# Kernel tuning notes

Hardware: AMD Instinct MI355X
Metric: run time of the kernel (lower is better)

## Reference

```python
import jax, jax.numpy as jnp
import numpy as np

N, E, D = 10000, 160000, 512


def setup_inputs() -> dict:
    key = jax.random.key(0)
    ks = jax.random.split(key, 5)
    x = jax.random.normal(ks[0], (N, D), dtype=jnp.float32)
    edge_index = jax.random.randint(ks[1], (2, E), 0, N, dtype=jnp.int32)
    W = jax.random.normal(ks[2], (D, D), dtype=jnp.float32) * (1.0 / np.sqrt(D))
    a_src = jax.random.normal(ks[3], (D,), dtype=jnp.float32) * 0.1
    a_dst = jax.random.normal(ks[4], (D,), dtype=jnp.float32) * 0.1
    bias = jnp.zeros((D,), dtype=jnp.float32)
    return {"x": x, "edge_index": edge_index, "W": W,
            "a_src": a_src, "a_dst": a_dst, "bias": bias}


def reference(x, edge_index, W, a_src, a_dst, bias):
    n = x.shape[0]
    # PyG GATConv default: add self-loops
    loops = jnp.arange(n, dtype=edge_index.dtype)
    src = jnp.concatenate([edge_index[0], loops])  # [E+N]
    dst = jnp.concatenate([edge_index[1], loops])  # [E+N]

    h = x @ W.T                                    # [N, D] linear projection
    e_src = h @ a_src                              # [N]
    e_dst = h @ a_dst                              # [N]
    e = e_src[src] + e_dst[dst]                    # [E+N]
    neg_slope = 0.2
    e = jnp.where(e > 0, e, neg_slope * e)         # leaky_relu

    # per-destination softmax (stable); self-loops guarantee non-empty segments
    m = jax.ops.segment_max(e, dst, num_segments=n)
    e = jnp.exp(e - m[dst])
    s = jax.ops.segment_sum(e, dst, num_segments=n)
    alpha = e / s[dst]                             # [E+N]

    msg = alpha[:, None] * h[src]                  # [E+N, D]
    out = jax.ops.segment_sum(msg, dst, num_segments=n) + bias  # [N, D]

    # module forward: x + elu(gat(x, edge_index))
    return x + jax.nn.elu(out)
```

## Files before the change

### kernel.cpp

```cpp
#include <hip/hip_runtime.h>
#include <hip/hip_bf16.h>

using bf16x8 = __attribute__((ext_vector_type(8))) __bf16;
using f32x4  = __attribute__((ext_vector_type(4))) float;

#define DFEAT 512
#define SLOTS 64

static __device__ __forceinline__ unsigned short f2bfbits(float f) {
    union { float f; unsigned int u; } v; v.f = f;
    unsigned int u = v.u;
    unsigned int r = (u + 0x7fffu + ((u >> 16) & 1u)) >> 16;
    return (unsigned short)r;
}

__global__ __launch_bounds__(256) void cvt_scatter_kernel(
    const float* __restrict__ x, const float* __restrict__ w,
    unsigned short* __restrict__ Xb, unsigned short* __restrict__ Wb,
    const int* __restrict__ srcv, const int* __restrict__ dstv,
    int* __restrict__ cur, int* __restrict__ slot,
    int nx4, int ntot4, int E, int T)
{
    int i = blockIdx.x * 256 + threadIdx.x;
    if (i < ntot4) {
        const float* in = (i < nx4) ? x : w;
        unsigned short* o = (i < nx4) ? Xb : Wb;
        int j = (i < nx4) ? i : i - nx4;
        float4 v = ((const float4*)in)[j];
        ushort4 u;
        u.x = f2bfbits(v.x); u.y = f2bfbits(v.y);
        u.z = f2bfbits(v.z); u.w = f2bfbits(v.w);
        ((ushort4*)o)[j] = u;
    }
    if (i < T) {
        int s, d;
        if (i < E) { s = srcv[i]; d = dstv[i]; }
        else       { s = d = i - E; }
        int pos = atomicAdd(&cur[d], 1);
        if (pos < SLOTS) slot[(size_t)d * SLOTS + pos] = s;
    }
}

__global__ __launch_bounds__(256, 2) void gemm_h_kernel(
    const unsigned short* __restrict__ X, const unsigned short* __restrict__ Wm,
    const float* __restrict__ avs, const float* __restrict__ avd,
    unsigned short* __restrict__ H, float* __restrict__ es, float* __restrict__ ed,
    int N)
{
    __shared__ unsigned short Bl[64 * 512];

    int L = blockIdx.x;
    int xcd = L & 7;
    int j   = L >> 3;
    int rpan = (j >> 3) * 8 + xcd;
    int cpan = j & 7;
    int rowPanels = (N + 127) >> 7;
    if (rpan >= rowPanels) return;
    int bm = rpan * 128;
    int bn = cpan * 64;

    int tid  = threadIdx.x;
    int wave = tid >> 6;
    int lane = tid & 63;
    int l15  = lane & 15;
    int quad = lane >> 4;

    for (int idx = tid; idx < 64 * 64; idx += 256) {
        int n = idx >> 6, c = idx & 63;
        uint4 v = *(const uint4*)(Wm + (size_t)(bn + n) * DFEAT + c * 8);
        int cs = c ^ (n & 7);
        *(uint4*)((char*)Bl + (size_t)n * 1024 + cs * 16) = v;
    }
    __syncthreads();

    int r0 = bm + wave * 32 + l15;
    int r1 = r0 + 16;
    int ra0 = r0 < N ? r0 : N - 1;
    int ra1 = r1 < N ? r1 : N - 1;
    const bf16x8* A0 = (const bf16x8*)(X + (size_t)ra0 * DFEAT);
    const bf16x8* A1 = (const bf16x8*)(X + (size_t)ra1 * DFEAT);
    const char* Bc = (const char*)Bl;
    int xorm = l15 & 7;
    int roff0 = (0 * 16 + l15) * 1024;
    int roff1 = (1 * 16 + l15) * 1024;
    int roff2 = (2 * 16 + l15) * 1024;
    int roff3 = (3 * 16 + l15) * 1024;

    f32x4 acc[2][4] = {};

    bf16x8 a0c = A0[quad],     a1c = A1[quad];
    bf16x8 a0n = A0[4 + quad], a1n = A1[4 + quad];
    bf16x8 b[4];
    {
        int cb = ((quad ^ xorm) * 16);
        b[0] = *(const bf16x8*)(Bc + roff0 + cb);
        b[1] = *(const bf16x8*)(Bc + roff1 + cb);
        b[2] = *(const bf16x8*)(Bc + roff2 + cb);
        b[3] = *(const bf16x8*)(Bc + roff3 + cb);
    }

    for (int k0 = 0; k0 < 16; ++k0) {
        int ka = ((k0 + 2 < 16 ? k0 + 2 : 15) * 4) + quad;
        bf16x8 a0f = A0[ka];
        bf16x8 a1f = A1[ka];
        int kb = ((k0 + 1 < 16 ? k0 + 1 : 15) * 4) + quad;
        int cb = (kb ^ xorm) * 16;
        bf16x8 bn0 = *(const bf16x8*)(Bc + roff0 + cb);
        bf16x8 bn1 = *(const bf16x8*)(Bc + roff1 + cb);
        bf16x8 bn2 = *(const bf16x8*)(Bc + roff2 + cb);
        bf16x8 bn3 = *(const bf16x8*)(Bc + roff3 + cb);
        acc[0][0] = __builtin_amdgcn_mfma_f32_16x16x32_bf16(a0c, b[0], acc[0][0], 0, 0, 0);
        acc[1][0] = __builtin_amdgcn_mfma_f32_16x16x32_bf16(a1c, b[0], acc[1][0], 0, 0, 0);
        acc[0][1] = __builtin_amdgcn_mfma_f32_16x16x32_bf16(a0c, b[1], acc[0][1], 0, 0, 0);
        acc[1][1] = __builtin_amdgcn_mfma_f32_16x16x32_bf16(a1c, b[1], acc[1][1], 0, 0, 0);
        acc[0][2] = __builtin_amdgcn_mfma_f32_16x16x32_bf16(a0c, b[2], acc[0][2], 0, 0, 0);
        acc[1][2] = __builtin_amdgcn_mfma_f32_16x16x32_bf16(a1c, b[2], acc[1][2], 0, 0, 0);
        acc[0][3] = __builtin_amdgcn_mfma_f32_16x16x32_bf16(a0c, b[3], acc[0][3], 0, 0, 0);
        acc[1][3] = __builtin_amdgcn_mfma_f32_16x16x32_bf16(a1c, b[3], acc[1][3], 0, 0, 0);
        a0c = a0n; a1c = a1n; a0n = a0f; a1n = a1f;
        b[0] = bn0; b[1] = bn1; b[2] = bn2; b[3] = bn3;
    }

    float as[4], ad[4];
    #pragma unroll
    for (int nt = 0; nt < 4; ++nt) {
        as[nt] = avs[bn + nt * 16 + l15];
        ad[nt] = avd[bn + nt * 16 + l15];
    }

    #pragma unroll
    for (int mt = 0; mt < 2; ++mt) {
        int rbase = bm + wave * 32 + mt * 16 + quad * 4;
        #pragma unroll
        for (int nt = 0; nt < 4; ++nt) {
            int col = bn + nt * 16 + l15;
            #pragma unroll
            for (int r = 0; r < 4; ++r) {
                int row = rbase + r;
                if (row < N) H[(size_t)row * DFEAT + col] = f2bfbits(acc[mt][nt][r]);
            }
        }
        #pragma unroll
        for (int r = 0; r < 4; ++r) {
            float ps = acc[mt][0][r] * as[0] + acc[mt][1][r] * as[1]
                     + acc[mt][2][r] * as[2] + acc[mt][3][r] * as[3];
            float pd = acc[mt][0][r] * ad[0] + acc[mt][1][r] * ad[1]
                     + acc[mt][2][r] * ad[2] + acc[mt][3][r] * ad[3];
            #pragma unroll
            for (int m = 1; m < 16; m <<= 1) {
                ps += __shfl_xor(ps, m);
                pd += __shfl_xor(pd, m);
            }
            int row = rbase + r;
            if (l15 == 0 && row < N) {
                atomicAdd(&es[row], ps);
                atomicAdd(&ed[row], pd);
            }
        }
    }
}

__global__ __launch_bounds__(256) void aggregate_kernel(
    const unsigned short* __restrict__ H, const float* __restrict__ x,
    const float* __restrict__ bias,
    const int* __restrict__ cur, const int* __restrict__ slot,
    const float* __restrict__ es, const float* __restrict__ ed,
    float* __restrict__ out, int N)
{
    int node = (blockIdx.x * 256 + threadIdx.x) >> 6;
    int lane = threadIdx.x & 63;
    if (node >= N) return;

    int k = cur[node];
    if (k > SLOTS) k = SLOTS;

    int   s = 0;
    float w = 0.f;
    if (lane < k) {
        s = slot[(size_t)node * SLOTS + lane];
        float e = es[s] + ed[node];
        e = e > 0.f ? e : 0.2f * e;
        w = __expf(e);
    }
    float denom = w;
    #pragma unroll
    for (int off = 32; off > 0; off >>= 1) denom += __shfl_xor(denom, off);
    float inv = 1.0f / denom;

    float a[8] = {};
    const unsigned short* Hl = H + lane * 8;

    auto accum = [&](int sj, float wj) {
        uint4 hv = *(const uint4*)(Hl + (size_t)sj * DFEAT);
        a[0] += wj * __uint_as_float(hv.x << 16);
        a[1] += wj * __uint_as_float(hv.x & 0xffff0000u);
        a[2] += wj * __uint_as_float(hv.y << 16);
        a[3] += wj * __uint_as_float(hv.y & 0xffff0000u);
        a[4] += wj * __uint_as_float(hv.z << 16);
        a[5] += wj * __uint_as_float(hv.z & 0xffff0000u);
        a[6] += wj * __uint_as_float(hv.w << 16);
        a[7] += wj * __uint_as_float(hv.w & 0xffff0000u);
    };

    int j = 0;
    for (; j + 3 < k; j += 4) {
        int   s0 = __shfl(s, j),     s1 = __shfl(s, j + 1);
        int   s2 = __shfl(s, j + 2), s3 = __shfl(s, j + 3);
        float w0 = __shfl(w, j),     w1 = __shfl(w, j + 1);
        float w2 = __shfl(w, j + 2), w3 = __shfl(w, j + 3);
        uint4 h0 = *(const uint4*)(Hl + (size_t)s0 * DFEAT);
        uint4 h1 = *(const uint4*)(Hl + (size_t)s1 * DFEAT);
        uint4 h2 = *(const uint4*)(Hl + (size_t)s2 * DFEAT);
        uint4 h3 = *(const uint4*)(Hl + (size_t)s3 * DFEAT);
        a[0] += w0 * __uint_as_float(h0.x << 16);
        a[1] += w0 * __uint_as_float(h0.x & 0xffff0000u);
        a[2] += w0 * __uint_as_float(h0.y << 16);
        a[3] += w0 * __uint_as_float(h0.y & 0xffff0000u);
        a[4] += w0 * __uint_as_float(h0.z << 16);
        a[5] += w0 * __uint_as_float(h0.z & 0xffff0000u);
        a[6] += w0 * __uint_as_float(h0.w << 16);
        a[7] += w0 * __uint_as_float(h0.w & 0xffff0000u);
        a[0] += w1 * __uint_as_float(h1.x << 16);
        a[1] += w1 * __uint_as_float(h1.x & 0xffff0000u);
        a[2] += w1 * __uint_as_float(h1.y << 16);
        a[3] += w1 * __uint_as_float(h1.y & 0xffff0000u);
        a[4] += w1 * __uint_as_float(h1.z << 16);
        a[5] += w1 * __uint_as_float(h1.z & 0xffff0000u);
        a[6] += w1 * __uint_as_float(h1.w << 16);
        a[7] += w1 * __uint_as_float(h1.w & 0xffff0000u);
        a[0] += w2 * __uint_as_float(h2.x << 16);
        a[1] += w2 * __uint_as_float(h2.x & 0xffff0000u);
        a[2] += w2 * __uint_as_float(h2.y << 16);
        a[3] += w2 * __uint_as_float(h2.y & 0xffff0000u);
        a[4] += w2 * __uint_as_float(h2.z << 16);
        a[5] += w2 * __uint_as_float(h2.z & 0xffff0000u);
        a[6] += w2 * __uint_as_float(h2.w << 16);
        a[7] += w2 * __uint_as_float(h2.w & 0xffff0000u);
        a[0] += w3 * __uint_as_float(h3.x << 16);
        a[1] += w3 * __uint_as_float(h3.x & 0xffff0000u);
        a[2] += w3 * __uint_as_float(h3.y << 16);
        a[3] += w3 * __uint_as_float(h3.y & 0xffff0000u);
        a[4] += w3 * __uint_as_float(h3.z << 16);
        a[5] += w3 * __uint_as_float(h3.z & 0xffff0000u);
        a[6] += w3 * __uint_as_float(h3.w << 16);
        a[7] += w3 * __uint_as_float(h3.w & 0xffff0000u);
    }
    for (; j < k; ++j) accum(__shfl(s, j), __shfl(w, j));

    int c = lane * 8;
    float4 b0 = *(const float4*)(bias + c);
    float4 b1 = *(const float4*)(bias + c + 4);
    float4 x0 = *(const float4*)(x + (size_t)node * DFEAT + c);
    float4 x1 = *(const float4*)(x + (size_t)node * DFEAT + c + 4);
    float r[8];
    r[0] = a[0] * inv + b0.x; r[1] = a[1] * inv + b0.y;
    r[2] = a[2] * inv + b0.z; r[3] = a[3] * inv + b0.w;
    r[4] = a[4] * inv + b1.x; r[5] = a[5] * inv + b1.y;
    r[6] = a[6] * inv + b1.z; r[7] = a[7] * inv + b1.w;
    #pragma unroll
    for (int i = 0; i < 8; ++i)
        r[i] = r[i] > 0.f ? r[i] : __expf(r[i]) - 1.f;
    float4 o0 = make_float4(x0.x + r[0], x0.y + r[1], x0.z + r[2], x0.w + r[3]);
    float4 o1 = make_float4(x1.x + r[4], x1.y + r[5], x1.z + r[6], x1.w + r[7]);
    *(float4*)(out + (size_t)node * DFEAT + c)     = o0;
    *(float4*)(out + (size_t)node * DFEAT + c + 4) = o1;
}

extern "C" void kernel_launch(void* const* d_in, const int* in_sizes, int n_in,
                              void* d_out, int out_size, void* d_ws, size_t ws_size,
                              hipStream_t stream)
{
    const float* x    = (const float*)d_in[0];
    const int*   edge = (const int*)d_in[1];
    const float* Wm   = (const float*)d_in[2];
    const float* avs  = (const float*)d_in[3];
    const float* avd  = (const float*)d_in[4];
    const float* bias = (const float*)d_in[5];

    const int D = DFEAT;
    const int N = in_sizes[0] / D;
    const int E = in_sizes[1] / 2;
    const int T = E + N;
    const int* srcv = edge;
    const int* dstv = edge + E;

    char* ws = (char*)d_ws;
    size_t off = 0;
    auto alloc = [&](size_t bytes) -> char* {
        char* p = ws + off;
        off += (bytes + 255) & ~(size_t)255;
        return p;
    };
    int*   cur  = (int*)alloc((size_t)N * 3 * 4);
    float* es   = (float*)(cur + N);
    float* ed   = es + N;
    int*   slot = (int*)alloc((size_t)N * SLOTS * 4);
    unsigned short* Xb = (unsigned short*)alloc((size_t)N * D * 2);
    unsigned short* Wb = (unsigned short*)alloc((size_t)D * D * 2);
    unsigned short* H  = (unsigned short*)alloc((size_t)N * D * 2);

    hipMemsetAsync(cur, 0, (size_t)N * 3 * 4, stream);

    int nx4   = (N * D) / 4;
    int ntot4 = nx4 + (D * D) / 4;
    int grid0 = (ntot4 > T ? ntot4 : T);
    cvt_scatter_kernel<<<dim3((grid0 + 255) / 256), 256, 0, stream>>>(
        x, Wm, Xb, Wb, srcv, dstv, cur, slot, nx4, ntot4, E, T);

    int rowPanels  = (N + 127) / 128;
    int rowPanels8 = ((rowPanels + 7) / 8) * 8;
    gemm_h_kernel<<<dim3(rowPanels8 * 8), 256, 0, stream>>>(
        Xb, Wb, avs, avd, H, es, ed, N);
    aggregate_kernel<<<dim3((N * 64 + 255) / 256), 256, 0, stream>>>(
        H, x, bias, cur, slot, es, ed, (float*)d_out, N);
}
```

Measured before the change: 144.8 us.

## Fuse bf16 conversion into GEMM and run edge scatter in extra GEMM blocks

Removes the separate convert/scatter kernel. The GEMM now reads fp32 X and W directly and converts them to bf16 in registers, so the bf16 staging copies of X and W are no longer written or read. The edge-slot scatter runs in extra blocks appended to the GEMM grid, which saves a launch and lets the atomics overlap with the matrix multiply. In exchange, the GEMM streams twice the bytes of A per tile, needs more registers to hold the fp32 prefetch buffers, and repeats the W conversion in every block.

```diff
diff --git a/kernel.cpp b/kernel.cpp
--- a/kernel.cpp
+++ b/kernel.cpp
@@ -14,42 +14,40 @@
     return (unsigned short)r;
 }
 
-__global__ __launch_bounds__(256) void cvt_scatter_kernel(
-    const float* __restrict__ x, const float* __restrict__ w,
-    unsigned short* __restrict__ Xb, unsigned short* __restrict__ Wb,
+static __device__ __forceinline__ bf16x8 cvt8(float4 u, float4 v) {
+    bf16x8 r;
+    r[0] = (__bf16)u.x; r[1] = (__bf16)u.y; r[2] = (__bf16)u.z; r[3] = (__bf16)u.w;
+    r[4] = (__bf16)v.x; r[5] = (__bf16)v.y; r[6] = (__bf16)v.z; r[7] = (__bf16)v.w;
+    return r;
+}
+
+__global__ __launch_bounds__(256, 2) void gemm_scatter_kernel(
+    const float* __restrict__ X, const float* __restrict__ Wf,
+    const float* __restrict__ avs, const float* __restrict__ avd,
+    unsigned short* __restrict__ H, float* __restrict__ es, float* __restrict__ ed,
     const int* __restrict__ srcv, const int* __restrict__ dstv,
     int* __restrict__ cur, int* __restrict__ slot,
-    int nx4, int ntot4, int E, int T)
-{
-    int i = blockIdx.x * 256 + threadIdx.x;
-    if (i < ntot4) {
-        const float* in = (i < nx4) ? x : w;
-        unsigned short* o = (i < nx4) ? Xb : Wb;
-        int j = (i < nx4) ? i : i - nx4;
-        float4 v = ((const float4*)in)[j];
-        ushort4 u;
-        u.x = f2bfbits(v.x); u.y = f2bfbits(v.y);
-        u.z = f2bfbits(v.z); u.w = f2bfbits(v.w);
-        ((ushort4*)o)[j] = u;
-    }
-    if (i < T) {
-        int s, d;
-        if (i < E) { s = srcv[i]; d = dstv[i]; }
-        else       { s = d = i - E; }
-        int pos = atomicAdd(&cur[d], 1);
-        if (pos < SLOTS) slot[(size_t)d * SLOTS + pos] = s;
-    }
-}
-
-__global__ __launch_bounds__(256, 2) void gemm_h_kernel(
-    const unsigned short* __restrict__ X, const unsigned short* __restrict__ Wm,
-    const float* __restrict__ avs, const float* __restrict__ avd,
-    unsigned short* __restrict__ H, float* __restrict__ es, float* __restrict__ ed,
-    int N)
+    int N, int E, int T, int Ggemm)
 {
     __shared__ unsigned short Bl[64 * 512];
 
     int L = blockIdx.x;
+    if (L >= Ggemm) {
+        int base = (L - Ggemm) * 1024 + threadIdx.x;
+        #pragma unroll
+        for (int t = 0; t < 4; ++t) {
+            int i = base + t * 256;
+            if (i < T) {
+                int s, d;
+                if (i < E) { s = srcv[i]; d = dstv[i]; }
+                else       { s = d = i - E; }
+                int pos = atomicAdd(&cur[d], 1);
+                if (pos < SLOTS) slot[(size_t)d * SLOTS + pos] = s;
+            }
+        }
+        return;
+    }
+
     int xcd = L & 7;
     int j   = L >> 3;
     int rpan = (j >> 3) * 8 + xcd;
@@ -67,9 +65,12 @@
 
     for (int idx = tid; idx < 64 * 64; idx += 256) {
         int n = idx >> 6, c = idx & 63;
-        uint4 v = *(const uint4*)(Wm + (size_t)(bn + n) * DFEAT + c * 8);
+        const float* wp = Wf + (size_t)(bn + n) * DFEAT + c * 8;
+        float4 u = *(const float4*)wp;
+        float4 v = *(const float4*)(wp + 4);
+        bf16x8 o = cvt8(u, v);
         int cs = c ^ (n & 7);
-        *(uint4*)((char*)Bl + (size_t)n * 1024 + cs * 16) = v;
+        *(bf16x8*)((char*)Bl + (size_t)n * 1024 + cs * 16) = o;
     }
     __syncthreads();
 
@@ -77,8 +78,8 @@
     int r1 = r0 + 16;
     int ra0 = r0 < N ? r0 : N - 1;
     int ra1 = r1 < N ? r1 : N - 1;
-    const bf16x8* A0 = (const bf16x8*)(X + (size_t)ra0 * DFEAT);
-    const bf16x8* A1 = (const bf16x8*)(X + (size_t)ra1 * DFEAT);
+    const float* A0p = X + (size_t)ra0 * DFEAT;
+    const float* A1p = X + (size_t)ra1 * DFEAT;
     const char* Bc = (const char*)Bl;
     int xorm = l15 & 7;
     int roff0 = (0 * 16 + l15) * 1024;
@@ -88,8 +89,15 @@
 
     f32x4 acc[2][4] = {};
 
-    bf16x8 a0c = A0[quad],     a1c = A1[quad];
-    bf16x8 a0n = A0[4 + quad], a1n = A1[4 + quad];
+    float4 c0u = *(const float4*)(A0p + quad * 8);
+    float4 c0v = *(const float4*)(A0p + quad * 8 + 4);
+    float4 c1u = *(const float4*)(A1p + quad * 8);
+    float4 c1v = *(const float4*)(A1p + quad * 8 + 4);
+    float4 n0u = *(const float4*)(A0p + (4 + quad) * 8);
+    float4 n0v = *(const float4*)(A0p + (4 + quad) * 8 + 4);
+    float4 n1u = *(const float4*)(A1p + (4 + quad) * 8);
+    float4 n1v = *(const float4*)(A1p + (4 + quad) * 8 + 4);
+
     bf16x8 b[4];
     {
         int cb = ((quad ^ xorm) * 16);
@@ -99,26 +107,55 @@
         b[3] = *(const bf16x8*)(Bc + roff3 + cb);
     }
 
-    for (int k0 = 0; k0 < 16; ++k0) {
-        int ka = ((k0 + 2 < 16 ? k0 + 2 : 15) * 4) + quad;
-        bf16x8 a0f = A0[ka];
-        bf16x8 a1f = A1[ka];
-        int kb = ((k0 + 1 < 16 ? k0 + 1 : 15) * 4) + quad;
-        int cb = (kb ^ xorm) * 16;
-        bf16x8 bn0 = *(const bf16x8*)(Bc + roff0 + cb);
-        bf16x8 bn1 = *(const bf16x8*)(Bc + roff1 + cb);
-        bf16x8 bn2 = *(const bf16x8*)(Bc + roff2 + cb);
-        bf16x8 bn3 = *(const bf16x8*)(Bc + roff3 + cb);
-        acc[0][0] = __builtin_amdgcn_mfma_f32_16x16x32_bf16(a0c, b[0], acc[0][0], 0, 0, 0);
-        acc[1][0] = __builtin_amdgcn_mfma_f32_16x16x32_bf16(a1c, b[0], acc[1][0], 0, 0, 0);
-        acc[0][1] = __builtin_amdgcn_mfma_f32_16x16x32_bf16(a0c, b[1], acc[0][1], 0, 0, 0);
-        acc[1][1] = __builtin_amdgcn_mfma_f32_16x16x32_bf16(a1c, b[1], acc[1][1], 0, 0, 0);
-        acc[0][2] = __builtin_amdgcn_mfma_f32_16x16x32_bf16(a0c, b[2], acc[0][2], 0, 0, 0);
-        acc[1][2] = __builtin_amdgcn_mfma_f32_16x16x32_bf16(a1c, b[2], acc[1][2], 0, 0, 0);
-        acc[0][3] = __builtin_amdgcn_mfma_f32_16x16x32_bf16(a0c, b[3], acc[0][3], 0, 0, 0);
-        acc[1][3] = __builtin_amdgcn_mfma_f32_16x16x32_bf16(a1c, b[3], acc[1][3], 0, 0, 0);
-        a0c = a0n; a1c = a1n; a0n = a0f; a1n = a1f;
-        b[0] = bn0; b[1] = bn1; b[2] = bn2; b[3] = bn3;
+    for (int k0 = 0; k0 < 16; k0 += 2) {
+        {
+            bf16x8 a0 = cvt8(c0u, c0v);
+            bf16x8 a1 = cvt8(c1u, c1v);
+            int ka = ((k0 + 2 < 16 ? k0 + 2 : 15) * 4 + quad) * 8;
+            c0u = *(const float4*)(A0p + ka);
+            c0v = *(const float4*)(A0p + ka + 4);
+            c1u = *(const float4*)(A1p + ka);
+            c1v = *(const float4*)(A1p + ka + 4);
+            int kb = (k0 + 1) * 4 + quad;
+            int cb = (kb ^ xorm) * 16;
+            bf16x8 bn0 = *(const bf16x8*)(Bc + roff0 + cb);
+            bf16x8 bn1 = *(const bf16x8*)(Bc + roff1 + cb);
+            bf16x8 bn2 = *(const bf16x8*)(Bc + roff2 + cb);
+            bf16x8 bn3 = *(const bf16x8*)(Bc + roff3 + cb);
+            acc[0][0] = __builtin_amdgcn_mfma_f32_16x16x32_bf16(a0, b[0], acc[0][0], 0, 0, 0);
+            acc[1][0] = __builtin_amdgcn_mfma_f32_16x16x32_bf16(a1, b[0], acc[1][0], 0, 0, 0);
+            acc[0][1] = __builtin_amdgcn_mfma_f32_16x16x32_bf16(a0, b[1], acc[0][1], 0, 0, 0);
+            acc[1][1] = __builtin_amdgcn_mfma_f32_16x16x32_bf16(a1, b[1], acc[1][1], 0, 0, 0);
+            acc[0][2] = __builtin_amdgcn_mfma_f32_16x16x32_bf16(a0, b[2], acc[0][2], 0, 0, 0);
+            acc[1][2] = __builtin_amdgcn_mfma_f32_16x16x32_bf16(a1, b[2], acc[1][2], 0, 0, 0);
+            acc[0][3] = __builtin_amdgcn_mfma_f32_16x16x32_bf16(a0, b[3], acc[0][3], 0, 0, 0);
+            acc[1][3] = __builtin_amdgcn_mfma_f32_16x16x32_bf16(a1, b[3], acc[1][3], 0, 0, 0);
+            b[0] = bn0; b[1] = bn1; b[2] = bn2; b[3] = bn3;
+        }
+        {
+            bf16x8 a0 = cvt8(n0u, n0v);
+            bf16x8 a1 = cvt8(n1u, n1v);
+            int ka = ((k0 + 3 < 16 ? k0 + 3 : 15) * 4 + quad) * 8;
+            n0u = *(const float4*)(A0p + ka);
+            n0v = *(const float4*)(A0p + ka + 4);
+            n1u = *(const float4*)(A1p + ka);
+            n1v = *(const float4*)(A1p + ka + 4);
+            int kb = (k0 + 2 < 16 ? k0 + 2 : 15) * 4 + quad;
+            int cb = (kb ^ xorm) * 16;
+            bf16x8 bn0 = *(const bf16x8*)(Bc + roff0 + cb);
+            bf16x8 bn1 = *(const bf16x8*)(Bc + roff1 + cb);
+            bf16x8 bn2 = *(const bf16x8*)(Bc + roff2 + cb);
+            bf16x8 bn3 = *(const bf16x8*)(Bc + roff3 + cb);
+            acc[0][0] = __builtin_amdgcn_mfma_f32_16x16x32_bf16(a0, b[0], acc[0][0], 0, 0, 0);
+            acc[1][0] = __builtin_amdgcn_mfma_f32_16x16x32_bf16(a1, b[0], acc[1][0], 0, 0, 0);
+            acc[0][1] = __builtin_amdgcn_mfma_f32_16x16x32_bf16(a0, b[1], acc[0][1], 0, 0, 0);
+            acc[1][1] = __builtin_amdgcn_mfma_f32_16x16x32_bf16(a1, b[1], acc[1][1], 0, 0, 0);
+            acc[0][2] = __builtin_amdgcn_mfma_f32_16x16x32_bf16(a0, b[2], acc[0][2], 0, 0, 0);
+            acc[1][2] = __builtin_amdgcn_mfma_f32_16x16x32_bf16(a1, b[2], acc[1][2], 0, 0, 0);
+            acc[0][3] = __builtin_amdgcn_mfma_f32_16x16x32_bf16(a0, b[3], acc[0][3], 0, 0, 0);
+            acc[1][3] = __builtin_amdgcn_mfma_f32_16x16x32_bf16(a1, b[3], acc[1][3], 0, 0, 0);
+            b[0] = bn0; b[1] = bn1; b[2] = bn2; b[3] = bn3;
+        }
     }
 
     float as[4], ad[4];
@@ -295,22 +332,17 @@
     float* es   = (float*)(cur + N);
     float* ed   = es + N;
     int*   slot = (int*)alloc((size_t)N * SLOTS * 4);
-    unsigned short* Xb = (unsigned short*)alloc((size_t)N * D * 2);
-    unsigned short* Wb = (unsigned short*)alloc((size_t)D * D * 2);
     unsigned short* H  = (unsigned short*)alloc((size_t)N * D * 2);
 
     hipMemsetAsync(cur, 0, (size_t)N * 3 * 4, stream);
-
-    int nx4   = (N * D) / 4;
-    int ntot4 = nx4 + (D * D) / 4;
-    int grid0 = (ntot4 > T ? ntot4 : T);
-    cvt_scatter_kernel<<<dim3((grid0 + 255) / 256), 256, 0, stream>>>(
-        x, Wm, Xb, Wb, srcv, dstv, cur, slot, nx4, ntot4, E, T);
 
     int rowPanels  = (N + 127) / 128;
     int rowPanels8 = ((rowPanels + 7) / 8) * 8;
-    gemm_h_kernel<<<dim3(rowPanels8 * 8), 256, 0, stream>>>(
-        Xb, Wb, avs, avd, H, es, ed, N);
+    int Ggemm = rowPanels8 * 8;
+    int Gscat = (T + 1023) / 1024;
+    gemm_scatter_kernel<<<dim3(Ggemm + Gscat), 256, 0, stream>>>(
+        x, Wm, avs, avd, H, es, ed, srcv, dstv, cur, slot, N, E, T, Ggemm);
+
     aggregate_kernel<<<dim3((N * 64 + 255) / 256), 256, 0, stream>>>(
         H, x, bias, cur, slot, es, ed, (float*)d_out, N);
 }
```

After: 146.3 us. No clear change (+1.1%).
